# Kernel optimization log

Hardware: AMD Instinct MI355X
Metric: run time of the kernel (lower is better)

The kernel has to match this reference:

```python
import jax, jax.numpy as jnp
import numpy as np

D_MODEL = 1024
N_HEADS = 16
D_K = D_MODEL // N_HEADS


def setup_inputs() -> dict:
    key = jax.random.key(0)
    ks = jax.random.split(key, 12)
    B, S, D, H = 2, 2048, D_MODEL, N_HEADS
    s = 1.0 / np.sqrt(D)
    inp = {
        "x": jax.random.normal(ks[0], (B, S, D), jnp.float32),
        "Wq": jax.random.normal(ks[1], (D, D), jnp.float32) * s,
        "bq": jnp.zeros((D,), jnp.float32),
        "Wk": jax.random.normal(ks[2], (D, D), jnp.float32) * s,
        "bk": jnp.zeros((D,), jnp.float32),
        "Wv": jax.random.normal(ks[3], (D, D), jnp.float32) * s,
        "bv": jnp.zeros((D,), jnp.float32),
        "Wo": jax.random.normal(ks[4], (D, D), jnp.float32) * s,
        "bo": jnp.zeros((D,), jnp.float32),
        "Wp": jax.random.normal(ks[5], (D, H), jnp.float32) * s,
        "bp": jnp.zeros((H,), jnp.float32),
        "alpha": jax.random.normal(ks[6], (H,), jnp.float32) * 0.1,
    }
    return inp


def reference(x, Wq, bq, Wk, bk, Wv, bv, Wo, bo, Wp, bp, alpha):
    B, S, D = x.shape
    H, dk = N_HEADS, D_K
    scale = dk ** -0.5
    # projections -> (B, H, S, dk)
    Q = (x @ Wq + bq).reshape(B, S, H, dk).transpose(0, 2, 1, 3)
    K = (x @ Wk + bk).reshape(B, S, H, dk).transpose(0, 2, 1, 3)
    V = (x @ Wv + bv).reshape(B, S, H, dk).transpose(0, 2, 1, 3)
    scores = jnp.einsum("bhid,bhjd->bhij", Q, K) * scale  # (B,H,S,S)
    # phase derived from x: (B,S,H) -> (B,H,S)
    phase = (x @ Wp + bp).transpose(0, 2, 1)
    # coherence(i,j) = cos(phi_i - phi_j), per batch/head
    coherence = jnp.cos(phase[:, :, :, None] - phase[:, :, None, :])
    scores = scores + alpha[None, :, None, None] * coherence
    attn = jax.nn.softmax(scores, axis=-1)
    out = jnp.einsum("bhij,bhjd->bhid", attn, V)  # (B,H,S,dk)
    out = out.transpose(0, 2, 1, 3).reshape(B, S, D)
    return out @ Wo + bo
```

## Files before the change

kernel.cpp:

```cpp
#include <hip/hip_runtime.h>
#include <math.h>


#define S_LEN 2048
#define NHEADS 16

typedef __attribute__((ext_vector_type(8))) short short8;
typedef __attribute__((ext_vector_type(4))) float floatx4;
typedef __attribute__((ext_vector_type(16))) float floatx16;

__device__ inline unsigned short f2bf(float f) {
    union { float f; unsigned int i; } v; v.f = f;
    unsigned int u = v.i;
    return (unsigned short)((u + 0x7fffu + ((u >> 16) & 1u)) >> 16);
}
__device__ inline unsigned int pack2_bf16(float hi, float lo) {
    union { float f; unsigned int u; } a, b; a.f = hi; b.f = lo;
    return __builtin_amdgcn_perm(a.u, b.u, 0x07060302u);
}
__device__ inline void async_copy16(const unsigned short* src, unsigned short* dst_lds) {
    __builtin_amdgcn_global_load_lds(
        (const __attribute__((address_space(1))) unsigned int*)(src),
        (__attribute__((address_space(3))) unsigned int*)(dst_lds), 16, 0, 0);
}
__device__ inline floatx16 zero16() {
    floatx16 v;
#pragma unroll
    for (int i = 0; i < 16; i++) v[i] = 0.f;
    return v;
}

__global__ __launch_bounds__(256) void prep_kernel(
    const float* __restrict__ x, const float* __restrict__ Wp,
    const float* __restrict__ bp, const float* __restrict__ alpha,
    const float* __restrict__ w0, const float* __restrict__ w1,
    const float* __restrict__ w2, const float* __restrict__ w3,
    unsigned short* __restrict__ d0, unsigned short* __restrict__ d1,
    unsigned short* __restrict__ d2, unsigned short* __restrict__ d3,
    unsigned short* __restrict__ qcs, unsigned short* __restrict__ kcs,
    unsigned short* __restrict__ xb) {
    __shared__ __align__(16) unsigned short shmem[64 * 72];
    int t = threadIdx.x;
    if (blockIdx.x < 4096) {
        float* red = reinterpret_cast<float*>(shmem);
        int bid = blockIdx.x;
        int b = bid >> 11, s = bid & 2047;
        int h = t & 15, c = t >> 4;
        const float* xr = x + (size_t)bid * 1024;
        {
            float4 xv = *reinterpret_cast<const float4*>(&xr[t * 4]);
            uint2 o;
            o.x = (unsigned int)f2bf(xv.x) | ((unsigned int)f2bf(xv.y) << 16);
            o.y = (unsigned int)f2bf(xv.z) | ((unsigned int)f2bf(xv.w) << 16);
            *reinterpret_cast<uint2*>(&xb[(size_t)bid * 1024 + t * 4]) = o;
        }
        float acc = 0.f;
#pragma unroll 8
        for (int kk = 0; kk < 64; kk++) {
            int k = c * 64 + kk;
            acc += xr[k] * Wp[k * 16 + h];
        }
        red[t] = acc;
        __syncthreads();
        if (t < 16) {
            float sum = 0.f;
#pragma unroll
            for (int c2 = 0; c2 < 16; c2++) sum += red[c2 * 16 + t];
            sum += bp[t];
            float sv, cv;
            __sincosf(sum, &sv, &cv);
            float as = alpha[t] * 1.44269504f;
            size_t off = ((size_t)(b * NHEADS + t) * S_LEN + s) * 16;
            uint4 qv = make_uint4(
                (unsigned int)f2bf(as * cv) | ((unsigned int)f2bf(as * sv) << 16), 0u, 0u, 0u);
            uint4 kv = make_uint4(
                (unsigned int)f2bf(cv) | ((unsigned int)f2bf(sv) << 16), 0u, 0u, 0u);
            uint4 z = make_uint4(0u, 0u, 0u, 0u);
            *reinterpret_cast<uint4*>(&qcs[off]) = qv;
            *reinterpret_cast<uint4*>(&qcs[off + 8]) = z;
            *reinterpret_cast<uint4*>(&kcs[off]) = kv;
            *reinterpret_cast<uint4*>(&kcs[off + 8]) = z;
        }
    } else {
        unsigned short (*tile)[72] = reinterpret_cast<unsigned short (*)[72]>(shmem);
        int bid = blockIdx.x - 4096;
        int mat = bid >> 8;
        int tl  = bid & 255;
        int tr = tl >> 4, tc = tl & 15;
        const float* src    = (mat == 0) ? w0 : (mat == 1) ? w1 : (mat == 2) ? w2 : w3;
        unsigned short* dst = (mat == 0) ? d0 : (mat == 1) ? d1 : (mat == 2) ? d2 : d3;
        int col = t & 63, rbase = (t >> 6) * 16;
#pragma unroll
        for (int i = 0; i < 16; i++) {
            int row = rbase + i;
            tile[row][col] = f2bf(src[(size_t)(tr * 64 + row) * 1024 + tc * 64 + col]);
        }
        __syncthreads();
#pragma unroll
        for (int i = 0; i < 16; i++) {
            int row = rbase + i;
            dst[(size_t)(tc * 64 + row) * 1024 + tr * 64 + col] = tile[col][row];
        }
    }
}

template <int MT>
__global__ __launch_bounds__(256) void gemm_bt(
    const unsigned short* __restrict__ A, const unsigned short* __restrict__ BT,
    int N, int mode,
    const float* __restrict__ b0, const float* __restrict__ b1,
    const float* __restrict__ b2,
    unsigned short* __restrict__ o0, unsigned short* __restrict__ o1,
    unsigned short* __restrict__ o2, float* __restrict__ of) {
    __shared__ __align__(16) unsigned short As[MT * 64];
    __shared__ __align__(16) unsigned short Bs[128 * 64];
    const int K = 1024;
    const int MI = MT / 32;
    int t = threadIdx.x;
    int mBase = blockIdx.x * MT;
    int nBase = blockIdx.y * 128;
    int w = t >> 6, lane = t & 63, l15 = lane & 15, quad = lane >> 4;
    int wm = (w & 1) * (MT / 2), wn = (w >> 1) * 64;
    floatx4 acc[MI][4];
#pragma unroll
    for (int i = 0; i < MI; i++)
#pragma unroll
        for (int j = 0; j < 4; j++) acc[i][j] = (floatx4){0.f, 0.f, 0.f, 0.f};

    int srow = t >> 3, sseg = t & 7;
    int scol = ((sseg - (srow & 7)) & 7) * 8;
    int rotf = l15 & 7;

    for (int k0 = 0; k0 < K; k0 += 64) {
        __syncthreads();
#pragma unroll
        for (int i = 0; i < MT / 32; i++)
            async_copy16(&A[(size_t)(mBase + i * 32 + srow) * K + k0 + scol],
                         &As[i * 2048 + t * 8]);
#pragma unroll
        for (int i = 0; i < 4; i++)
            async_copy16(&BT[(size_t)(nBase + i * 32 + srow) * K + k0 + scol],
                         &Bs[i * 2048 + t * 8]);
        __syncthreads();
#pragma unroll
        for (int kk = 0; kk < 2; kk++) {
            int gr = ((kk * 4 + quad + rotf) & 7) * 8;
            short8 af[MI], bfr[4];
#pragma unroll
            for (int mi = 0; mi < MI; mi++)
                af[mi] = *reinterpret_cast<const short8*>(&As[(wm + mi * 16 + l15) * 64 + gr]);
#pragma unroll
            for (int ni = 0; ni < 4; ni++)
                bfr[ni] = *reinterpret_cast<const short8*>(&Bs[(wn + ni * 16 + l15) * 64 + gr]);
#pragma unroll
            for (int mi = 0; mi < MI; mi++)
#pragma unroll
                for (int ni = 0; ni < 4; ni++)
                    acc[mi][ni] = __builtin_amdgcn_mfma_f32_16x16x32_bf16(af[mi], bfr[ni], acc[mi][ni], 0, 0, 0);
        }
    }

#pragma unroll
    for (int mi = 0; mi < MI; mi++) {
        int rowB = mBase + wm + mi * 16 + quad * 4;
#pragma unroll
        for (int ni = 0; ni < 4; ni++) {
            int col = nBase + wn + ni * 16 + l15;
            if (mode == 0) {
                float bias = b0[col];
#pragma unroll
                for (int r = 0; r < 4; r++) {
                    of[(size_t)(rowB + r) * N + col] = acc[mi][ni][r] + bias;
                }
            } else {
                int mat = col >> 10, nn = col & 1023;
                int h = nn >> 6, d = nn & 63;
                int b = rowB >> 11, sidx = rowB & 2047;
                if (mat == 2) {
                    float bv = b2[nn];
                    unsigned int lo = (unsigned int)f2bf(acc[mi][ni][0] + bv) |
                                      ((unsigned int)f2bf(acc[mi][ni][1] + bv) << 16);
                    unsigned int hi = (unsigned int)f2bf(acc[mi][ni][2] + bv) |
                                      ((unsigned int)f2bf(acc[mi][ni][3] + bv) << 16);
                    int jj = sidx & 15;
                    int s23 = ((jj & 4) << 1) | ((jj & 8) >> 1);
                    size_t rowOff = ((size_t)((b * NHEADS + h) * 64 + d)) * S_LEN +
                                    (sidx & ~15) + s23;
                    *reinterpret_cast<uint2*>(&o2[rowOff]) = make_uint2(lo, hi);
                } else {
                    const float* bias  = (mat == 0) ? b0 : b1;
                    unsigned short* op = (mat == 0) ? o0 : o1;
                    float bv = bias[nn];
                    float scl = (mat == 0) ? 0.18033688f : 1.0f;
#pragma unroll
                    for (int r = 0; r < 4; r++) {
                        float cv = (acc[mi][ni][r] + bv) * scl;
                        op[(((size_t)b * NHEADS + h) * S_LEN + (sidx + r)) * 64 + d] = f2bf(cv);
                    }
                }
            }
        }
    }
}

__global__ __launch_bounds__(512, 4) void attn_kernel(
    const unsigned short* __restrict__ Qg, const unsigned short* __restrict__ Qcs,
    const unsigned short* __restrict__ Kg, const unsigned short* __restrict__ Kcs,
    const unsigned short* __restrict__ VTg, unsigned short* __restrict__ ctx) {
    __shared__ __align__(16) unsigned short smem[36864];

    int bid = blockIdx.x;
    int bh = bid >> 4, qt = bid & 15;
    int t = threadIdx.x, lane = t & 63;
    int half = t >> 8, th = t & 255;
    int cg = (t >> 6) & 3;
    int l31 = lane & 31, g = lane >> 5;
    int i0w = qt * 128 + cg * 32;
    size_t base = (size_t)bh * (S_LEN * 64);
    size_t basec = (size_t)bh * (S_LEN * 16);

    short8 qd[4], qc;
    {
        const unsigned short* qrow = Qg + base + (size_t)(i0w + l31) * 64;
#pragma unroll
        for (int f = 0; f < 4; f++)
            qd[f] = *reinterpret_cast<const short8*>(qrow + f * 16 + g * 8);
        qc = *reinterpret_cast<const short8*>(Qcs + basec + (size_t)(i0w + l31) * 16 + g * 8);
    }

    int srow = th >> 3, sseg = th & 7;
    int scol = ((sseg - (srow & 7)) & 7) * 8;
    const unsigned short* kd0 = Kg + base + (size_t)srow * 64 + scol;
    const unsigned short* kd1 = Kg + base + (size_t)(srow + 32) * 64 + scol;
    const unsigned short* vv0 = VTg + base + (size_t)srow * S_LEN + scol;
    const unsigned short* vv1 = VTg + base + (size_t)(srow + 32) * S_LEN + scol;
    const unsigned short* kcc = Kcs + basec + th * 8;

    unsigned short* KD0 = smem + (half * 2) * 4096;
    unsigned short* KD1 = smem + (half * 2 + 1) * 4096;
    unsigned short* VT0 = smem + 16384 + (half * 2) * 4096;
    unsigned short* VT1 = smem + 16384 + (half * 2 + 1) * 4096;
    unsigned short* KC0 = smem + 32768 + (half * 2) * 1024;
    unsigned short* KC1 = smem + 32768 + (half * 2 + 1) * 1024;

    int kt0 = half * 16;
    {
        async_copy16(kd0 + (size_t)kt0 * 4096, KD0 + th * 8);
        async_copy16(kd1 + (size_t)kt0 * 4096, KD0 + 2048 + th * 8);
        async_copy16(vv0 + kt0 * 64, VT0 + th * 8);
        async_copy16(vv1 + kt0 * 64, VT0 + 2048 + th * 8);
        if (th < 128) async_copy16(kcc + (size_t)kt0 * 1024, KC0 + th * 8);
    }

    floatx16 o0 = zero16(), o1 = zero16(), lac = zero16();
    const short8 ones8 = {(short)0x3F80, (short)0x3F80, (short)0x3F80, (short)0x3F80,
                          (short)0x3F80, (short)0x3F80, (short)0x3F80, (short)0x3F80};

    int rot = l31 & 7;
    int kcof = l31 * 16 + g * 8;
    int arow = l31 * 64;

    for (int it = 0; it < 16; it++) {
        int p = it & 1;
        unsigned short* KDp = p ? KD1 : KD0;
        unsigned short* VTp = p ? VT1 : VT0;
        unsigned short* KCp = p ? KC1 : KC0;
        __syncthreads();
        if (it < 15) {
            int kn = kt0 + it + 1;
            unsigned short* KDn = p ? KD0 : KD1;
            unsigned short* VTn = p ? VT0 : VT1;
            unsigned short* KCn = p ? KC0 : KC1;
            async_copy16(kd0 + (size_t)kn * 4096, KDn + th * 8);
            async_copy16(kd1 + (size_t)kn * 4096, KDn + 2048 + th * 8);
            async_copy16(vv0 + kn * 64, VTn + th * 8);
            async_copy16(vv1 + kn * 64, VTn + 2048 + th * 8);
            if (th < 128) async_copy16(kcc + (size_t)kn * 1024, KCn + th * 8);
        }

        short8 pf[4];
#pragma unroll
        for (int jt = 0; jt < 2; jt++) {
            const unsigned short* kb = KDp + jt * 2048 + arow;
            floatx16 st = zero16();
#pragma unroll
            for (int f = 0; f < 4; f++) {
                int fo = ((2 * f + g + rot) & 7) * 8;
                st = __builtin_amdgcn_mfma_f32_32x32x16_bf16(
                    *reinterpret_cast<const short8*>(kb + fo), qd[f], st, 0, 0, 0);
            }
            st = __builtin_amdgcn_mfma_f32_32x32x16_bf16(
                *reinterpret_cast<const short8*>(KCp + jt * 512 + kcof), qc, st, 0, 0, 0);
            float pe[16];
#pragma unroll
            for (int r = 0; r < 16; r++) pe[r] = __builtin_amdgcn_exp2f(st[r]);
#pragma unroll
            for (int h = 0; h < 2; h++) {
                union { unsigned int u[4]; short8 s; } pk;
                pk.u[0] = pack2_bf16(pe[8 * h + 1], pe[8 * h + 0]);
                pk.u[1] = pack2_bf16(pe[8 * h + 3], pe[8 * h + 2]);
                pk.u[2] = pack2_bf16(pe[8 * h + 5], pe[8 * h + 4]);
                pk.u[3] = pack2_bf16(pe[8 * h + 7], pe[8 * h + 6]);
                pf[2 * jt + h] = pk.s;
            }
        }

#pragma unroll
        for (int c = 0; c < 4; c++) {
            lac = __builtin_amdgcn_mfma_f32_32x32x16_bf16(pf[c], ones8, lac, 0, 0, 0);
            int vo = ((2 * c + g + rot) & 7) * 8;
            short8 vf0 = *reinterpret_cast<const short8*>(VTp + arow + vo);
            short8 vf1 = *reinterpret_cast<const short8*>(VTp + 2048 + arow + vo);
            o0 = __builtin_amdgcn_mfma_f32_32x32x16_bf16(pf[c], vf0, o0, 0, 0, 0);
            o1 = __builtin_amdgcn_mfma_f32_32x32x16_bf16(pf[c], vf1, o1, 0, 0, 0);
        }
    }

    float* xch = reinterpret_cast<float*>(smem);
    __syncthreads();
    if (half == 1) {
        int xb2 = cg * 3072 + lane;
#pragma unroll
        for (int r = 0; r < 16; r++) {
            xch[xb2 + r * 64]        = o0[r];
            xch[xb2 + (16 + r) * 64] = o1[r];
            xch[xb2 + (32 + r) * 64] = lac[r];
        }
    }
    __syncthreads();
    if (half == 0) {
        int xb2 = cg * 3072 + lane;
#pragma unroll
        for (int r = 0; r < 16; r++) {
            o0[r] += xch[xb2 + r * 64];
            o1[r] += xch[xb2 + (16 + r) * 64];
            lac[r] += xch[xb2 + (32 + r) * 64];
        }
        int b = bh >> 4, h = bh & 15;
#pragma unroll
        for (int r = 0; r < 16; r++) {
            int i = i0w + (r & 3) + 8 * (r >> 2) + 4 * g;
            float inv = 1.0f / lac[r];
            size_t off = ((size_t)(b * S_LEN + i)) * 1024 + h * 64;
            ctx[off + l31]      = f2bf(o0[r] * inv);
            ctx[off + 32 + l31] = f2bf(o1[r] * inv);
        }
    }
}

extern "C" void kernel_launch(void* const* d_in, const int* in_sizes, int n_in,
                              void* d_out, int out_size, void* d_ws, size_t ws_size,
                              hipStream_t stream) {
    const float* x     = (const float*)d_in[0];
    const float* Wq    = (const float*)d_in[1];
    const float* bq    = (const float*)d_in[2];
    const float* Wk    = (const float*)d_in[3];
    const float* bk    = (const float*)d_in[4];
    const float* Wv    = (const float*)d_in[5];
    const float* bv    = (const float*)d_in[6];
    const float* Wo    = (const float*)d_in[7];
    const float* bo    = (const float*)d_in[8];
    const float* Wp    = (const float*)d_in[9];
    const float* bp    = (const float*)d_in[10];
    const float* alpha = (const float*)d_in[11];
    float* out = (float*)d_out;

    const size_t MB = 1048576;
    char* ws = (char*)d_ws;
    unsigned short* WT   = (unsigned short*)(ws);
    unsigned short* WoT  = (unsigned short*)(ws + 6 * MB);
    unsigned short* xb   = (unsigned short*)(ws + 8 * MB);
    unsigned short* ctx  = (unsigned short*)(ws + 8 * MB);
    unsigned short* Qw   = (unsigned short*)(ws + 16 * MB);
    unsigned short* Kw   = (unsigned short*)(ws + 24 * MB);
    unsigned short* VTg  = (unsigned short*)(ws + 32 * MB);
    unsigned short* Qcs  = (unsigned short*)(ws + 40 * MB);
    unsigned short* Kcs  = (unsigned short*)(ws + 42 * MB);

    prep_kernel<<<dim3(5120), dim3(256), 0, stream>>>(
        x, Wp, bp, alpha, Wq, Wk, Wv, Wo,
        WT, WT + 1048576, WT + 2097152, WoT, Qcs, Kcs, xb);
    gemm_bt<128><<<dim3(32, 24), dim3(256), 0, stream>>>(
        xb, WT, 3072, 1, bq, bk, bv, Qw, Kw, VTg, (float*)nullptr);
    attn_kernel<<<dim3(512), dim3(512), 0, stream>>>(
        Qw, Qcs, Kw, Kcs, VTg, ctx);
    gemm_bt<64><<<dim3(64, 8), dim3(256), 0, stream>>>(
        ctx, WoT, 1024, 0, bo, bo, bo,
        (unsigned short*)nullptr, (unsigned short*)nullptr,
        (unsigned short*)nullptr, out);
}
```

Before: 224.3 us.

## Load GEMM MFMA fragments directly from global memory with register double-buffering

Both projection GEMMs stop staging A and B tiles through shared memory with async copies and barriers. Each lane now loads its 16-byte MFMA fragments straight from global memory, prefetching the next k-step into a second register buffer while the current one is multiplied. This removes LDS traffic and the two __syncthreads per k-tile. In exchange each wave re-reads operands that other waves in the block share, so it depends on L1/L2 for reuse and adds register pressure.

```diff
diff --git a/kernel.cpp b/kernel.cpp
--- a/kernel.cpp
+++ b/kernel.cpp
@@ -105,15 +105,13 @@
 }
 
 template <int MT>
-__global__ __launch_bounds__(256) void gemm_bt(
+__global__ __launch_bounds__(256) void gemm_rr(
     const unsigned short* __restrict__ A, const unsigned short* __restrict__ BT,
     int N, int mode,
     const float* __restrict__ b0, const float* __restrict__ b1,
     const float* __restrict__ b2,
     unsigned short* __restrict__ o0, unsigned short* __restrict__ o1,
     unsigned short* __restrict__ o2, float* __restrict__ of) {
-    __shared__ __align__(16) unsigned short As[MT * 64];
-    __shared__ __align__(16) unsigned short Bs[128 * 64];
     const int K = 1024;
     const int MI = MT / 32;
     int t = threadIdx.x;
@@ -127,37 +125,35 @@
 #pragma unroll
         for (int j = 0; j < 4; j++) acc[i][j] = (floatx4){0.f, 0.f, 0.f, 0.f};
 
-    int srow = t >> 3, sseg = t & 7;
-    int scol = ((sseg - (srow & 7)) & 7) * 8;
-    int rotf = l15 & 7;
-
-    for (int k0 = 0; k0 < K; k0 += 64) {
-        __syncthreads();
-#pragma unroll
-        for (int i = 0; i < MT / 32; i++)
-            async_copy16(&A[(size_t)(mBase + i * 32 + srow) * K + k0 + scol],
-                         &As[i * 2048 + t * 8]);
-#pragma unroll
-        for (int i = 0; i < 4; i++)
-            async_copy16(&BT[(size_t)(nBase + i * 32 + srow) * K + k0 + scol],
-                         &Bs[i * 2048 + t * 8]);
-        __syncthreads();
-#pragma unroll
-        for (int kk = 0; kk < 2; kk++) {
-            int gr = ((kk * 4 + quad + rotf) & 7) * 8;
-            short8 af[MI], bfr[4];
+    const unsigned short* aPtr = A + (size_t)(mBase + wm + l15) * K + quad * 8;
+    const unsigned short* bPtr = BT + (size_t)(nBase + wn + l15) * K + quad * 8;
+
+    short8 af[2][MI], bfr[2][4];
+#pragma unroll
+    for (int mi = 0; mi < MI; mi++)
+        af[0][mi] = *reinterpret_cast<const short8*>(aPtr + mi * 16 * K);
+#pragma unroll
+    for (int ni = 0; ni < 4; ni++)
+        bfr[0][ni] = *reinterpret_cast<const short8*>(bPtr + ni * 16 * K);
+
+#pragma unroll
+    for (int kk = 0; kk < 32; kk++) {
+        int p = kk & 1;
+        if (kk < 31) {
+            int off = (kk + 1) * 32;
 #pragma unroll
             for (int mi = 0; mi < MI; mi++)
-                af[mi] = *reinterpret_cast<const short8*>(&As[(wm + mi * 16 + l15) * 64 + gr]);
+                af[p ^ 1][mi] = *reinterpret_cast<const short8*>(aPtr + mi * 16 * K + off);
 #pragma unroll
             for (int ni = 0; ni < 4; ni++)
-                bfr[ni] = *reinterpret_cast<const short8*>(&Bs[(wn + ni * 16 + l15) * 64 + gr]);
-#pragma unroll
-            for (int mi = 0; mi < MI; mi++)
-#pragma unroll
-                for (int ni = 0; ni < 4; ni++)
-                    acc[mi][ni] = __builtin_amdgcn_mfma_f32_16x16x32_bf16(af[mi], bfr[ni], acc[mi][ni], 0, 0, 0);
-        }
+                bfr[p ^ 1][ni] = *reinterpret_cast<const short8*>(bPtr + ni * 16 * K + off);
+        }
+#pragma unroll
+        for (int mi = 0; mi < MI; mi++)
+#pragma unroll
+            for (int ni = 0; ni < 4; ni++)
+                acc[mi][ni] = __builtin_amdgcn_mfma_f32_16x16x32_bf16(
+                    af[p][mi], bfr[p][ni], acc[mi][ni], 0, 0, 0);
     }
 
 #pragma unroll
@@ -380,11 +376,11 @@
     prep_kernel<<<dim3(5120), dim3(256), 0, stream>>>(
         x, Wp, bp, alpha, Wq, Wk, Wv, Wo,
         WT, WT + 1048576, WT + 2097152, WoT, Qcs, Kcs, xb);
-    gemm_bt<128><<<dim3(32, 24), dim3(256), 0, stream>>>(
+    gemm_rr<128><<<dim3(32, 24), dim3(256), 0, stream>>>(
         xb, WT, 3072, 1, bq, bk, bv, Qw, Kw, VTg, (float*)nullptr);
     attn_kernel<<<dim3(512), dim3(512), 0, stream>>>(
         Qw, Qcs, Kw, Kcs, VTg, ctx);
-    gemm_bt<64><<<dim3(64, 8), dim3(256), 0, stream>>>(
+    gemm_rr<64><<<dim3(64, 8), dim3(256), 0, stream>>>(
         ctx, WoT, 1024, 0, bo, bo, bo,
         (unsigned short*)nullptr, (unsigned short*)nullptr,
         (unsigned short*)nullptr, out);
```

Result: slower. 309.2 us (+37.8%).
